# Optimization experiments

Hardware: AMD Instinct MI355X
Metric: run time of the kernel (lower is better)

## Reference

```python
import jax, jax.numpy as jnp
import numpy as np

N_NODES = 100000
N_EDGES = 3200000
IN_DIM = 256
HID = 128
OUT = 2
BN_EPS = 1e-5


def setup_inputs() -> dict:
    key = jax.random.key(0)
    ks = jax.random.split(key, 4)
    x = jax.random.normal(ks[0], (N_NODES, IN_DIM), dtype=jnp.float32)
    edge_index = jax.random.randint(ks[1], (2, N_EDGES), 0, N_NODES, dtype=jnp.int64)
    # Glorot-ish scaled weights
    W1 = jax.random.normal(ks[2], (IN_DIM, HID), dtype=jnp.float32) * (1.0 / np.sqrt(IN_DIM))
    W2 = jax.random.normal(ks[3], (HID, OUT), dtype=jnp.float32) * (1.0 / np.sqrt(HID))
    return {
        "x": x,
        "edge_index": edge_index,
        "feature_importance": jnp.ones((IN_DIM,), jnp.float32),
        "W1": W1,
        "b1": jnp.zeros((HID,), jnp.float32),
        "W2": W2,
        "b2": jnp.zeros((OUT,), jnp.float32),
        "gamma": jnp.ones((HID,), jnp.float32),
        "beta": jnp.zeros((HID,), jnp.float32),
    }


def _gcn_conv(x, row, col, norm, W, b, n_nodes):
    # PyG GCNConv: linear transform then D^-1/2 (A+I) D^-1/2 aggregation
    h = x @ W  # [N, d_out]
    msg = h[row] * norm[:, None]  # gather + scale, [E+N, d_out]
    out = jax.ops.segment_sum(msg, col, num_segments=n_nodes)  # scatter-add
    return out + b


def _norm_and_loops(edge_index, n_nodes, dtype):
    loop = jnp.arange(n_nodes, dtype=edge_index.dtype)
    row = jnp.concatenate([edge_index[0], loop])
    col = jnp.concatenate([edge_index[1], loop])
    deg = jax.ops.segment_sum(jnp.ones_like(col, dtype=dtype), col, num_segments=n_nodes)
    dinv = jnp.where(deg > 0, jax.lax.rsqrt(deg), 0.0)
    norm = dinv[row] * dinv[col]
    return row, col, norm


def reference(x, edge_index, feature_importance, W1, b1, W2, b2, gamma, beta):
    n_nodes = x.shape[0]
    row, col, norm = _norm_and_loops(edge_index, n_nodes, x.dtype)
    # sigmoid feature-importance weighting
    xw = x * jax.nn.sigmoid(feature_importance)
    h = _gcn_conv(xw, row, col, norm, W1, b1, n_nodes)
    # BatchNorm1d with batch statistics (training-mode math; dropout omitted = eval)
    mu = jnp.mean(h, axis=0)
    var = jnp.mean((h - mu) ** 2, axis=0)
    h = (h - mu) * jax.lax.rsqrt(var + BN_EPS) * gamma + beta
    h = jax.nn.relu(h)
    out = _gcn_conv(h, row, col, norm, W2, b2, n_nodes)
    return out
```

## Files before the change

### kernel.cpp

```cpp
#include <hip/hip_runtime.h>
#include <hip/hip_bf16.h>

#define N_NODES 100000
#define N_EDGES 3200000
#define IN_DIM 256
#define HID 128
#define BN_EPS 1e-5f
#define SCAN_B 1024
#define NB1 ((N_NODES + SCAN_B - 1) / SCAN_B)

typedef __attribute__((ext_vector_type(8))) short bf16x8;
typedef __attribute__((ext_vector_type(4))) float f32x4;

__device__ __forceinline__ ushort f2bf(float f) {
    unsigned u = __float_as_uint(f);
    u += 0x7FFFu + ((u >> 16) & 1u);
    return (ushort)(u >> 16);
}
__device__ __forceinline__ float bflo(unsigned v) { return __uint_as_float(v << 16); }
__device__ __forceinline__ float bfhi(unsigned v) { return __uint_as_float(v & 0xFFFF0000u); }


__global__ void k_deg(const int* __restrict__ col, unsigned* __restrict__ cnt) {
    int i = blockIdx.x * blockDim.x + threadIdx.x;
    if (i < N_EDGES) atomicAdd(&cnt[col[i]], 1u);
}

__global__ void k_dinv(const unsigned* __restrict__ cnt, float* __restrict__ dinv) {
    int i = blockIdx.x * blockDim.x + threadIdx.x;
    if (i < N_NODES) dinv[i] = rsqrtf((float)(cnt[i] + 1u));
}

__global__ void k_sig(const float* __restrict__ fi, float* __restrict__ sig) {
    int i = threadIdx.x;
    if (i < IN_DIM) sig[i] = 1.0f / (1.0f + expf(-fi[i]));
}

__global__ void k_prepw(const float* __restrict__ W1, const float* __restrict__ sig,
                        ushort* __restrict__ W1t) {
    int idx = blockIdx.x * blockDim.x + threadIdx.x;
    if (idx < HID * IN_DIM) {
        int n = idx >> 8, k = idx & 255;
        W1t[idx] = f2bf(W1[k * HID + n] * sig[k]);
    }
}


__global__ __launch_bounds__(SCAN_B) void k_scan_part(const unsigned* __restrict__ cnt,
                                                      unsigned* __restrict__ rowptr,
                                                      unsigned* __restrict__ blocksum) {
    __shared__ unsigned s[SCAN_B];
    int t = threadIdx.x;
    int i = blockIdx.x * SCAN_B + t;
    unsigned v = (i < N_NODES) ? cnt[i] : 0u;
    s[t] = v;
    __syncthreads();
#pragma unroll
    for (int off = 1; off < SCAN_B; off <<= 1) {
        unsigned u = (t >= off) ? s[t - off] : 0u;
        __syncthreads();
        s[t] += u;
        __syncthreads();
    }
    if (i < N_NODES) rowptr[i] = s[t] - v;
    if (t == SCAN_B - 1) blocksum[blockIdx.x] = s[t];
}

__global__ __launch_bounds__(128) void k_scan_mid(const unsigned* __restrict__ blocksum,
                                                  unsigned* __restrict__ blockoff) {
    __shared__ unsigned s[128];
    int t = threadIdx.x;
    unsigned v = (t < NB1) ? blocksum[t] : 0u;
    s[t] = v;
    __syncthreads();
#pragma unroll
    for (int off = 1; off < 128; off <<= 1) {
        unsigned u = (t >= off) ? s[t - off] : 0u;
        __syncthreads();
        s[t] += u;
        __syncthreads();
    }
    if (t < NB1) blockoff[t] = s[t] - v;
}

__global__ void k_scan_add(unsigned* __restrict__ rowptr, const unsigned* __restrict__ blockoff) {
    int i = blockIdx.x * blockDim.x + threadIdx.x;
    if (i < N_NODES) rowptr[i] += blockoff[i >> 10];
    if (i == 0) rowptr[N_NODES] = N_EDGES;
}


__global__ void k_bucket(const int* __restrict__ row, const int* __restrict__ col,
                         const unsigned* __restrict__ rowptr, unsigned* __restrict__ fill,
                         int* __restrict__ esrc) {
    int e = blockIdx.x * blockDim.x + threadIdx.x;
    if (e < N_EDGES) {
        int c = col[e];
        unsigned p = rowptr[c] + atomicAdd(&fill[c], 1u);
        esrc[p] = row[e];
    }
}


__global__ __launch_bounds__(256) void k_gemm1(const float* __restrict__ x,
                                               const ushort* __restrict__ W1t,
                                               const float* __restrict__ dinv,
                                               unsigned* __restrict__ hsu) {
    const int t = threadIdx.x;
    const int w = (blockIdx.x << 2) + (t >> 6);
    const int m0 = w << 4;
    if (m0 >= N_NODES) return;
    const int lane = t & 63;
    const int mrow = lane & 15;
    const int quad = lane >> 4;

    const float* xrow = x + (size_t)(m0 + mrow) * IN_DIM + quad * 8;
    const ushort* wrow = W1t + mrow * IN_DIM + quad * 8;

    f32x4 acc[8] = {};
#pragma unroll
    for (int ks = 0; ks < 8; ++ks) {
        float4 xa = *(const float4*)(xrow + ks * 32);
        float4 xb = *(const float4*)(xrow + ks * 32 + 4);
        bf16x8 bfrag;
        bfrag[0] = (short)f2bf(xa.x); bfrag[1] = (short)f2bf(xa.y);
        bfrag[2] = (short)f2bf(xa.z); bfrag[3] = (short)f2bf(xa.w);
        bfrag[4] = (short)f2bf(xb.x); bfrag[5] = (short)f2bf(xb.y);
        bfrag[6] = (short)f2bf(xb.z); bfrag[7] = (short)f2bf(xb.w);
        const ushort* wk = wrow + ks * 32;
#pragma unroll
        for (int nb = 0; nb < 8; ++nb) {
            bf16x8 afrag = *(const bf16x8*)(wk + nb * 16 * IN_DIM);
            acc[nb] = __builtin_amdgcn_mfma_f32_16x16x32_bf16(afrag, bfrag, acc[nb], 0, 0, 0);
        }
    }
    const float d = dinv[m0 + mrow];
    unsigned* orow = hsu + (size_t)(m0 + mrow) * 64;
#pragma unroll
    for (int nb = 0; nb < 8; ++nb) {
        unsigned p0 = (unsigned)f2bf(acc[nb][0] * d) | ((unsigned)f2bf(acc[nb][1] * d) << 16);
        unsigned p1 = (unsigned)f2bf(acc[nb][2] * d) | ((unsigned)f2bf(acc[nb][3] * d) << 16);
        *(uint2*)(orow + nb * 8 + quad * 2) = make_uint2(p0, p1);
    }
}


__global__ __launch_bounds__(256) void k_agg1csr(const int* __restrict__ esrc,
                                                 const unsigned* __restrict__ rowptr,
                                                 const unsigned* __restrict__ hsu,
                                                 const float* __restrict__ dinv,
                                                 const float* __restrict__ b1,
                                                 float* __restrict__ S1,
                                                 float* __restrict__ stats) {
    const int t = threadIdx.x;
    const int lane = t & 63;
    const int gw = (blockIdx.x * blockDim.x + t) >> 6;
    const int nw = (gridDim.x * blockDim.x) >> 6;
    const int ch = lane * 2;
    const float2 bb = *(const float2*)&b1[ch];
    float s0 = 0.f, s1 = 0.f, q0 = 0.f, q1 = 0.f;

    for (int c = gw; c < N_NODES; c += nw) {
        unsigned beg = rowptr[c], end = rowptr[c + 1];
        unsigned self = hsu[(size_t)c * 64 + lane];
        float a0 = bflo(self), a1 = bfhi(self);
        for (unsigned base = beg; base < end; base += 64) {
            int n = (int)min(64u, end - base);
            int my = (lane < n) ? esrc[base + lane] : 0;
#pragma unroll 4
            for (int i = 0; i < n; ++i) {
                int r = __shfl(my, i);
                unsigned v = hsu[(size_t)r * 64 + lane];
                a0 += bflo(v); a1 += bfhi(v);
            }
        }
        float d = dinv[c];
        float v0 = d * a0 + bb.x;
        float v1 = d * a1 + bb.y;
        *(float2*)&S1[(size_t)c * HID + ch] = make_float2(v0, v1);
        s0 += v0; s1 += v1; q0 += v0 * v0; q1 += v1 * v1;
    }

    __shared__ float red[256];
#define RED_ATOMIC(val, idx)                                              \
    red[t] = (val); __syncthreads();                                      \
    if (t < 64) {                                                         \
        float r_ = red[t] + red[t + 64] + red[t + 128] + red[t + 192];    \
        atomicAdd(&stats[idx], r_);                                       \
    } __syncthreads();
    RED_ATOMIC(s0, ch)
    RED_ATOMIC(s1, ch + 1)
    RED_ATOMIC(q0, 128 + ch)
    RED_ATOMIC(q1, 129 + ch)
#undef RED_ATOMIC
}


__global__ void k_bnfin(const float* __restrict__ stats,
                        const float* __restrict__ gamma,
                        const float* __restrict__ beta,
                        float* __restrict__ bnp) {
    int j = threadIdx.x;
    if (j < HID) {
        float mu = stats[j] * (1.0f / N_NODES);
        float var = stats[128 + j] * (1.0f / N_NODES) - mu * mu;
        float rstd = rsqrtf(var + BN_EPS);
        float sc = rstd * gamma[j];
        bnp[j] = sc;
        bnp[128 + j] = beta[j] - mu * sc;
    }
}


__global__ __launch_bounds__(256) void k_gemm2(const float* __restrict__ S1,
                                               const float* __restrict__ bnp,
                                               const float* __restrict__ W2,
                                               const float* __restrict__ dinv,
                                               float* __restrict__ gs) {
    int wid = (blockIdx.x * blockDim.x + threadIdx.x) >> 6;
    int lane = threadIdx.x & 63;
    int nw = (gridDim.x * blockDim.x) >> 6;
    int k0 = lane * 2;
    float2 sc = *(const float2*)&bnp[k0];
    float2 sh = *(const float2*)&bnp[128 + k0];
    float4 w = *(const float4*)&W2[k0 * 2];
    for (int n = wid; n < N_NODES; n += nw) {
        float2 h = *(const float2*)&S1[(size_t)n * HID + k0];
        float v0 = fmaxf(h.x * sc.x + sh.x, 0.f);
        float v1 = fmaxf(h.y * sc.y + sh.y, 0.f);
        float a0 = v0 * w.x + v1 * w.z;
        float a1 = v0 * w.y + v1 * w.w;
#pragma unroll
        for (int off = 32; off; off >>= 1) {
            a0 += __shfl_down(a0, off);
            a1 += __shfl_down(a1, off);
        }
        if (lane == 0) {
            float d = dinv[n];
            *(float2*)&gs[n * 2] = make_float2(a0 * d, a1 * d);
        }
    }
}


__global__ void k_agg2csr(const int* __restrict__ esrc,
                          const unsigned* __restrict__ rowptr,
                          const float* __restrict__ gs,
                          const float* __restrict__ dinv,
                          const float* __restrict__ b2,
                          float* __restrict__ out) {
    int c = blockIdx.x * blockDim.x + threadIdx.x;
    if (c >= N_NODES) return;
    float2 acc = *(const float2*)&gs[c * 2];
    unsigned beg = rowptr[c], end = rowptr[c + 1];
    for (unsigned i = beg; i < end; ++i) {
        int r = esrc[i];
        float2 v = *(const float2*)&gs[r * 2];
        acc.x += v.x; acc.y += v.y;
    }
    float d = dinv[c];
    *(float2*)&out[c * 2] = make_float2(d * acc.x + b2[0], d * acc.y + b2[1]);
}


extern "C" void kernel_launch(void* const* d_in, const int* in_sizes, int n_in,
                              void* d_out, int out_size, void* d_ws, size_t ws_size,
                              hipStream_t stream) {
    const float* x     = (const float*)d_in[0];
    const int*   edge  = (const int*)d_in[1];
    const float* fi    = (const float*)d_in[2];
    const float* W1    = (const float*)d_in[3];
    const float* b1    = (const float*)d_in[4];
    const float* W2    = (const float*)d_in[5];
    const float* b2    = (const float*)d_in[6];
    const float* gamma = (const float*)d_in[7];
    const float* beta  = (const float*)d_in[8];
    float* out = (float*)d_out;

    const int* erow = edge;
    const int* ecol = edge + N_EDGES;

    char* ws = (char*)d_ws;
    size_t off = 0;
    auto alloc = [&](size_t bytes) { size_t r = off; off = (off + bytes + 255) & ~(size_t)255; return r; };
    unsigned* hsu   = (unsigned*)(ws + alloc(sizeof(unsigned) * (size_t)N_NODES * 64));
    float*    S1    = (float*)(ws + alloc(sizeof(float) * (size_t)N_NODES * HID));
    int*      esrc  = (int*)(ws + alloc(sizeof(int) * (size_t)N_EDGES));
    float*    gs    = (float*)(ws + alloc(sizeof(float) * N_NODES * 2));
    unsigned* cnt   = (unsigned*)(ws + alloc(sizeof(unsigned) * N_NODES));
    unsigned* fill  = (unsigned*)(ws + alloc(sizeof(unsigned) * N_NODES));
    unsigned* rowptr= (unsigned*)(ws + alloc(sizeof(unsigned) * (N_NODES + 1)));
    unsigned* bsum  = (unsigned*)(ws + alloc(sizeof(unsigned) * NB1));
    unsigned* boff  = (unsigned*)(ws + alloc(sizeof(unsigned) * NB1));
    float*    dinv  = (float*)(ws + alloc(sizeof(float) * N_NODES));
    float*    sig   = (float*)(ws + alloc(sizeof(float) * IN_DIM));
    ushort*   W1t   = (ushort*)(ws + alloc(sizeof(ushort) * HID * IN_DIM));
    float*    stats = (float*)(ws + alloc(sizeof(float) * 2 * HID));
    float*    bnp   = (float*)(ws + alloc(sizeof(float) * 2 * HID));
    (void)ws_size; (void)in_sizes; (void)n_in; (void)out_size;

    hipMemsetAsync(cnt, 0, sizeof(unsigned) * N_NODES, stream);
    hipMemsetAsync(fill, 0, sizeof(unsigned) * N_NODES, stream);
    hipMemsetAsync(stats, 0, sizeof(float) * 2 * HID, stream);

    k_deg<<<(N_EDGES + 255) / 256, 256, 0, stream>>>(ecol, cnt);
    k_dinv<<<(N_NODES + 255) / 256, 256, 0, stream>>>(cnt, dinv);
    k_sig<<<1, 256, 0, stream>>>(fi, sig);
    k_prepw<<<(HID * IN_DIM + 255) / 256, 256, 0, stream>>>(W1, sig, W1t);

    k_scan_part<<<NB1, SCAN_B, 0, stream>>>(cnt, rowptr, bsum);
    k_scan_mid<<<1, 128, 0, stream>>>(bsum, boff);
    k_scan_add<<<(N_NODES + 255) / 256, 256, 0, stream>>>(rowptr, boff);
    k_bucket<<<(N_EDGES + 255) / 256, 256, 0, stream>>>(erow, ecol, rowptr, fill, esrc);

    k_gemm1<<<(N_NODES / 16 + 3) / 4, 256, 0, stream>>>(x, W1t, dinv, hsu);
    k_agg1csr<<<2048, 256, 0, stream>>>(esrc, rowptr, hsu, dinv, b1, S1, stats);
    k_bnfin<<<1, 128, 0, stream>>>(stats, gamma, beta, bnp);
    k_gemm2<<<2048, 256, 0, stream>>>(S1, bnp, W2, dinv, gs);
    k_agg2csr<<<(N_NODES + 255) / 256, 256, 0, stream>>>(esrc, rowptr, gs, dinv, b2, out);
}
```

Baseline: 822.4 us.

## Store layer-1 output as bf16, fuse small prep kernels, unroll CSR gathers

Stores the layer-1 aggregated activations S1 as packed bf16 instead of fp32, halving the write and reread traffic between agg1 and gemm2. Folds the dinv computation into the scan kernel and the sigmoid into the weight-prep kernel, which removes two launches, and merges the two memsets into one. The CSR gather loops in both aggregation kernels now read edge indices directly with unrolling instead of wave-wide load-and-shuffle. The bf16 rounding of S1 adds some precision loss before BatchNorm is applied.

```diff
diff --git a/kernel.cpp b/kernel.cpp
--- a/kernel.cpp
+++ b/kernel.cpp
@@ -26,33 +26,26 @@
     if (i < N_EDGES) atomicAdd(&cnt[col[i]], 1u);
 }
 
-__global__ void k_dinv(const unsigned* __restrict__ cnt, float* __restrict__ dinv) {
-    int i = blockIdx.x * blockDim.x + threadIdx.x;
-    if (i < N_NODES) dinv[i] = rsqrtf((float)(cnt[i] + 1u));
-}
-
-__global__ void k_sig(const float* __restrict__ fi, float* __restrict__ sig) {
-    int i = threadIdx.x;
-    if (i < IN_DIM) sig[i] = 1.0f / (1.0f + expf(-fi[i]));
-}
-
-__global__ void k_prepw(const float* __restrict__ W1, const float* __restrict__ sig,
+__global__ void k_prepw(const float* __restrict__ W1, const float* __restrict__ fi,
                         ushort* __restrict__ W1t) {
     int idx = blockIdx.x * blockDim.x + threadIdx.x;
     if (idx < HID * IN_DIM) {
         int n = idx >> 8, k = idx & 255;
-        W1t[idx] = f2bf(W1[k * HID + n] * sig[k]);
+        float s = 1.0f / (1.0f + expf(-fi[k]));
+        W1t[idx] = f2bf(W1[k * HID + n] * s);
     }
 }
 
 
 __global__ __launch_bounds__(SCAN_B) void k_scan_part(const unsigned* __restrict__ cnt,
                                                       unsigned* __restrict__ rowptr,
-                                                      unsigned* __restrict__ blocksum) {
+                                                      unsigned* __restrict__ blocksum,
+                                                      float* __restrict__ dinv) {
     __shared__ unsigned s[SCAN_B];
     int t = threadIdx.x;
     int i = blockIdx.x * SCAN_B + t;
     unsigned v = (i < N_NODES) ? cnt[i] : 0u;
+    if (i < N_NODES) dinv[i] = rsqrtf((float)(v + 1u));
     s[t] = v;
     __syncthreads();
 #pragma unroll
@@ -150,7 +143,7 @@
                                                  const unsigned* __restrict__ hsu,
                                                  const float* __restrict__ dinv,
                                                  const float* __restrict__ b1,
-                                                 float* __restrict__ S1,
+                                                 unsigned* __restrict__ S1u,
                                                  float* __restrict__ stats) {
     const int t = threadIdx.x;
     const int lane = t & 63;
@@ -161,23 +154,27 @@
     float s0 = 0.f, s1 = 0.f, q0 = 0.f, q1 = 0.f;
 
     for (int c = gw; c < N_NODES; c += nw) {
-        unsigned beg = rowptr[c], end = rowptr[c + 1];
+        const unsigned beg = rowptr[c], end = rowptr[c + 1];
         unsigned self = hsu[(size_t)c * 64 + lane];
         float a0 = bflo(self), a1 = bfhi(self);
-        for (unsigned base = beg; base < end; base += 64) {
-            int n = (int)min(64u, end - base);
-            int my = (lane < n) ? esrc[base + lane] : 0;
-#pragma unroll 4
-            for (int i = 0; i < n; ++i) {
-                int r = __shfl(my, i);
+        unsigned i = beg;
+        for (; i + 8 <= end; i += 8) {
+#pragma unroll
+            for (int u = 0; u < 8; ++u) {
+                int r = esrc[i + u];
                 unsigned v = hsu[(size_t)r * 64 + lane];
                 a0 += bflo(v); a1 += bfhi(v);
             }
         }
+        for (; i < end; ++i) {
+            int r = esrc[i];
+            unsigned v = hsu[(size_t)r * 64 + lane];
+            a0 += bflo(v); a1 += bfhi(v);
+        }
         float d = dinv[c];
         float v0 = d * a0 + bb.x;
         float v1 = d * a1 + bb.y;
-        *(float2*)&S1[(size_t)c * HID + ch] = make_float2(v0, v1);
+        S1u[(size_t)c * 64 + lane] = (unsigned)f2bf(v0) | ((unsigned)f2bf(v1) << 16);
         s0 += v0; s1 += v1; q0 += v0 * v0; q1 += v1 * v1;
     }
 
@@ -212,7 +209,7 @@
 }
 
 
-__global__ __launch_bounds__(256) void k_gemm2(const float* __restrict__ S1,
+__global__ __launch_bounds__(256) void k_gemm2(const unsigned* __restrict__ S1u,
                                                const float* __restrict__ bnp,
                                                const float* __restrict__ W2,
                                                const float* __restrict__ dinv,
@@ -225,9 +222,9 @@
     float2 sh = *(const float2*)&bnp[128 + k0];
     float4 w = *(const float4*)&W2[k0 * 2];
     for (int n = wid; n < N_NODES; n += nw) {
-        float2 h = *(const float2*)&S1[(size_t)n * HID + k0];
-        float v0 = fmaxf(h.x * sc.x + sh.x, 0.f);
-        float v1 = fmaxf(h.y * sc.y + sh.y, 0.f);
+        unsigned hv = S1u[(size_t)n * 64 + lane];
+        float v0 = fmaxf(bflo(hv) * sc.x + sh.x, 0.f);
+        float v1 = fmaxf(bfhi(hv) * sc.y + sh.y, 0.f);
         float a0 = v0 * w.x + v1 * w.z;
         float a1 = v0 * w.y + v1 * w.w;
 #pragma unroll
@@ -253,7 +250,16 @@
     if (c >= N_NODES) return;
     float2 acc = *(const float2*)&gs[c * 2];
     unsigned beg = rowptr[c], end = rowptr[c + 1];
-    for (unsigned i = beg; i < end; ++i) {
+    unsigned i = beg;
+    for (; i + 4 <= end; i += 4) {
+#pragma unroll
+        for (int u = 0; u < 4; ++u) {
+            int r = esrc[i + u];
+            float2 v = *(const float2*)&gs[r * 2];
+            acc.x += v.x; acc.y += v.y;
+        }
+    }
+    for (; i < end; ++i) {
         int r = esrc[i];
         float2 v = *(const float2*)&gs[r * 2];
         acc.x += v.x; acc.y += v.y;
@@ -284,38 +290,34 @@
     size_t off = 0;
     auto alloc = [&](size_t bytes) { size_t r = off; off = (off + bytes + 255) & ~(size_t)255; return r; };
     unsigned* hsu   = (unsigned*)(ws + alloc(sizeof(unsigned) * (size_t)N_NODES * 64));
-    float*    S1    = (float*)(ws + alloc(sizeof(float) * (size_t)N_NODES * HID));
+    unsigned* S1u   = (unsigned*)(ws + alloc(sizeof(unsigned) * (size_t)N_NODES * 64));
     int*      esrc  = (int*)(ws + alloc(sizeof(int) * (size_t)N_EDGES));
     float*    gs    = (float*)(ws + alloc(sizeof(float) * N_NODES * 2));
-    unsigned* cnt   = (unsigned*)(ws + alloc(sizeof(unsigned) * N_NODES));
-    unsigned* fill  = (unsigned*)(ws + alloc(sizeof(unsigned) * N_NODES));
+    unsigned* cnt   = (unsigned*)(ws + alloc(sizeof(unsigned) * N_NODES * 2));
+    unsigned* fill  = cnt + N_NODES;
     unsigned* rowptr= (unsigned*)(ws + alloc(sizeof(unsigned) * (N_NODES + 1)));
     unsigned* bsum  = (unsigned*)(ws + alloc(sizeof(unsigned) * NB1));
     unsigned* boff  = (unsigned*)(ws + alloc(sizeof(unsigned) * NB1));
     float*    dinv  = (float*)(ws + alloc(sizeof(float) * N_NODES));
-    float*    sig   = (float*)(ws + alloc(sizeof(float) * IN_DIM));
     ushort*   W1t   = (ushort*)(ws + alloc(sizeof(ushort) * HID * IN_DIM));
     float*    stats = (float*)(ws + alloc(sizeof(float) * 2 * HID));
     float*    bnp   = (float*)(ws + alloc(sizeof(float) * 2 * HID));
     (void)ws_size; (void)in_sizes; (void)n_in; (void)out_size;
 
-    hipMemsetAsync(cnt, 0, sizeof(unsigned) * N_NODES, stream);
-    hipMemsetAsync(fill, 0, sizeof(unsigned) * N_NODES, stream);
+    hipMemsetAsync(cnt, 0, sizeof(unsigned) * N_NODES * 2, stream);
     hipMemsetAsync(stats, 0, sizeof(float) * 2 * HID, stream);
 
     k_deg<<<(N_EDGES + 255) / 256, 256, 0, stream>>>(ecol, cnt);
-    k_dinv<<<(N_NODES + 255) / 256, 256, 0, stream>>>(cnt, dinv);
-    k_sig<<<1, 256, 0, stream>>>(fi, sig);
-    k_prepw<<<(HID * IN_DIM + 255) / 256, 256, 0, stream>>>(W1, sig, W1t);
-
-    k_scan_part<<<NB1, SCAN_B, 0, stream>>>(cnt, rowptr, bsum);
+    k_prepw<<<(HID * IN_DIM + 255) / 256, 256, 0, stream>>>(W1, fi, W1t);
+
+    k_scan_part<<<NB1, SCAN_B, 0, stream>>>(cnt, rowptr, bsum, dinv);
     k_scan_mid<<<1, 128, 0, stream>>>(bsum, boff);
     k_scan_add<<<(N_NODES + 255) / 256, 256, 0, stream>>>(rowptr, boff);
     k_bucket<<<(N_EDGES + 255) / 256, 256, 0, stream>>>(erow, ecol, rowptr, fill, esrc);
 
     k_gemm1<<<(N_NODES / 16 + 3) / 4, 256, 0, stream>>>(x, W1t, dinv, hsu);
-    k_agg1csr<<<2048, 256, 0, stream>>>(esrc, rowptr, hsu, dinv, b1, S1, stats);
+    k_agg1csr<<<2048, 256, 0, stream>>>(esrc, rowptr, hsu, dinv, b1, S1u, stats);
     k_bnfin<<<1, 128, 0, stream>>>(stats, gamma, beta, bnp);
-    k_gemm2<<<2048, 256, 0, stream>>>(S1, bnp, W2, dinv, gs);
+    k_gemm2<<<2048, 256, 0, stream>>>(S1u, bnp, W2, dinv, gs);
     k_agg2csr<<<(N_NODES + 255) / 256, 256, 0, stream>>>(esrc, rowptr, gs, dinv, b2, out);
 }
```

After: 747.5 us. 9.1% less time.
